# Optimization experiments

Measured on AMD Instinct MI355X. Metric: run time of the kernel, lower is better.

The kernel has to match this reference:

```python
import jax, jax.numpy as jnp
import numpy as np

TGT, BSZ, E, H, HD, P = 256, 64, 1024, 16, 64, 16
TAU = 3.0  # gumbel temperature
SCALE = 1.0 / np.sqrt(HD)


def setup_inputs() -> dict:
    rng = jax.random.key(0)
    ks = jax.random.split(rng, 14)
    n = lambda i, s: jax.random.normal(ks[i], s, dtype=jnp.float32)
    u = jax.random.uniform(ks[7], (BSZ, 2), dtype=jnp.float32, minval=1e-6, maxval=1.0 - 1e-6)
    return {
        'idx': 0,
        'query': n(0, (TGT, BSZ, E)),
        'key': n(1, (TGT, BSZ, E)),
        'value': n(2, (TGT, BSZ, E)),
        'prefix': n(3, (BSZ, 2, P, E)) * 0.5,  # gathered prefix_pool[prompt_ids]
        'batch_weight': jax.random.uniform(ks[4], (BSZ,), dtype=jnp.float32),
        'ori_image_features': n(5, (BSZ, 512)),
        'gumbel_noise': -jnp.log(-jnp.log(u)),  # standard gumbel(0,1) noise
        'in_proj_w': n(8, (3 * E, E)) * 0.02,
        'in_proj_b': jnp.zeros((3 * E,), jnp.float32),
        'out_w': n(9, (E, E)) * 0.02,
        'out_b': jnp.zeros((E,), jnp.float32),
        'gumbel_w': n(10, (2, 512)) * 0.05,
        'gumbel_b': jnp.zeros((2,), jnp.float32),
    }


def _sdpa(q, k, v):
    # q:[b,h,t,d] k,v:[b,h,s,d]
    s = jnp.einsum('bhtd,bhsd->bhts', q, k) * SCALE
    a = jax.nn.softmax(s, axis=-1)
    return jnp.einsum('bhts,bhsd->bhtd', a, v)


def reference(idx, query, key, value, prefix, batch_weight, ori_image_features,
              gumbel_noise, in_proj_w, in_proj_b, out_w, out_b, gumbel_w, gumbel_b):
    tgt, bsz, e = query.shape
    src = key.shape[0]
    # packed in-projection (w chunked into q/k/v blocks)
    w_q, w_k, w_v = jnp.split(in_proj_w, 3, axis=0)
    b_q, b_k, b_v = jnp.split(in_proj_b, 3, axis=0)
    q = query @ w_q.T + b_q            # [t,b,E]
    k = key @ w_k.T + b_k              # [s,b,E]
    v = value @ w_v.T + b_v
    # -> [b,h,t,d]
    q = q.reshape(tgt, bsz, H, HD).transpose(1, 2, 0, 3)
    k = k.reshape(src, bsz, H, HD).transpose(1, 2, 0, 3)
    v = v.reshape(src, bsz, H, HD).transpose(1, 2, 0, 3)
    # prefix k/v: [b,P,E] -> [b,h,P,d] (no in-projection, used raw as in source)
    pk = prefix[:, 0].reshape(bsz, P, H, HD).transpose(0, 2, 1, 3)
    pv = prefix[:, 1].reshape(bsz, P, H, HD).transpose(0, 2, 1, 3)

    attn = _sdpa(q, k, v)                      # [b,h,t,d]
    attn_flat = attn.transpose(2, 0, 1, 3).reshape(tgt * bsz, e)  # (t,b) row order

    attn_pre = _sdpa(q, pk, pv) * batch_weight[:, None, None, None]
    attn_pre_flat = attn_pre.transpose(2, 0, 1, 3).reshape(tgt * bsz, e)

    # gumbel-softmax gate (soft), one 2-way gate per sample
    logits = ori_image_features @ gumbel_w.T + gumbel_b           # [b,2]
    gumbel = jax.nn.softmax((logits + gumbel_noise) / TAU, axis=-1)
    gate = jnp.repeat(gumbel, tgt, axis=0)                        # [b*t,2] (b,t) order, as in source
    combined = attn_flat * gate[:, :1] + (attn_flat + attn_pre_flat) * gate[:, 1:2]

    out = combined @ out_w.T + out_b
    return out.reshape(tgt, bsz, e)
```

## Files before the change

kernel.cpp:

```cpp
#include <hip/hip_runtime.h>

typedef __attribute__((ext_vector_type(8))) short bf16x8;
typedef __attribute__((ext_vector_type(4))) float f32x4;
typedef __attribute__((ext_vector_type(8))) unsigned short ushort8;
typedef __attribute__((ext_vector_type(4))) unsigned short ushort4v;
typedef __attribute__((ext_vector_type(4))) float float4v;
typedef __attribute__((ext_vector_type(2))) unsigned int uint2v;

#define TGT 256
#define BSZ 64
#define EMB 1024
#define NH 16
#define HD 64
#define PP 16

__device__ __forceinline__ float b2f(unsigned short u) {
  return __builtin_bit_cast(float, ((unsigned int)u) << 16);
}
__device__ __forceinline__ unsigned short f2b(float f) {
  unsigned int u = __builtin_bit_cast(unsigned int, f);
  u += 0x7fffu + ((u >> 16) & 1u);
  return (unsigned short)(u >> 16);
}
__device__ __forceinline__ unsigned int pack2(float lo, float hi) {
  return (unsigned int)f2b(lo) | ((unsigned int)f2b(hi) << 16);
}
__device__ __forceinline__ f32x4 mfma16(bf16x8 a, bf16x8 b, f32x4 c) {
  return __builtin_amdgcn_mfma_f32_16x16x32_bf16(a, b, c, 0, 0, 0);
}
__device__ __forceinline__ void gl_lds16(const unsigned short* g, unsigned short* l) {
  __builtin_amdgcn_global_load_lds(
      (const __attribute__((address_space(1))) unsigned int*)g,
      (__attribute__((address_space(3))) unsigned int*)l, 16, 0, 0);
}

__global__ __launch_bounds__(64) void gate_kernel(
    const float* __restrict__ feat, const float* __restrict__ gw,
    const float* __restrict__ gb, const float* __restrict__ noise,
    float* __restrict__ g1) {
  const int b = blockIdx.x, lane = threadIdx.x;
  float a0 = 0.f, a1 = 0.f;
  for (int i = lane; i < 512; i += 64) {
    float f = feat[b * 512 + i];
    a0 += f * gw[i];
    a1 += f * gw[512 + i];
  }
#pragma unroll
  for (int off = 32; off >= 1; off >>= 1) {
    a0 += __shfl_xor(a0, off);
    a1 += __shfl_xor(a1, off);
  }
  if (lane == 0) {
    float l0 = (a0 + gb[0] + noise[b * 2 + 0]) * (1.0f / 3.0f);
    float l1 = (a1 + gb[1] + noise[b * 2 + 1]) * (1.0f / 3.0f);
    float mm = fmaxf(l0, l1);
    float e0 = __expf(l0 - mm), e1 = __expf(l1 - mm);
    g1[b] = e1 / (e0 + e1);
  }
}

__global__ __launch_bounds__(256) void cast_bf16_kernel(
    const float* __restrict__ in, unsigned short* __restrict__ out, int n8) {
  int i = blockIdx.x * blockDim.x + threadIdx.x;
  const int stride = gridDim.x * blockDim.x;
  for (; i < n8; i += stride) {
    const float4v* p = (const float4v*)(in + (size_t)i * 8);
    float4v v0 = p[0], v1 = p[1];
    ushort8 o = {f2b(v0[0]), f2b(v0[1]), f2b(v0[2]), f2b(v0[3]),
                 f2b(v1[0]), f2b(v1[1]), f2b(v1[2]), f2b(v1[3])};
    *(ushort8*)(out + (size_t)i * 8) = o;
  }
}

#define STAGE_A(s)                                       \
  {                                                      \
    int k0s = (s) * 32;                                  \
    unsigned short* d = &As[(s) & 3][wl];                \
    gl_lds16(a0p + k0s, d);                              \
    gl_lds16(a1p + k0s, d + 4096);                       \
  }
#define STAGE_B(s)                                       \
  {                                                      \
    int k0s = (s) * 32;                                  \
    unsigned short* d = &Bs[(s) & 3][wl];                \
    gl_lds16(b0p + k0s, d);                              \
    gl_lds16(b1p + k0s, d + 4096);                       \
  }
#define GEMM_STEP(s, DO_STAGE)                                        \
  {                                                                   \
    const unsigned short* Ab = &As[(s) & 3][0];                       \
    const unsigned short* Bb = &Bs[(s) & 3][0];                       \
    bf16x8 af[8], bfr[4];                                             \
    _Pragma("unroll") for (int mi = 0; mi < 8; ++mi)                  \
        af[mi] = *(const bf16x8*)&Ab[aoff + mi * 512];                \
    _Pragma("unroll") for (int ni = 0; ni < 2; ++ni)                  \
        bfr[ni] = *(const bf16x8*)&Bb[boff + ni * 512];               \
    if (DO_STAGE) STAGE_A((s) + 3);                                   \
    __builtin_amdgcn_s_barrier();                                     \
    __builtin_amdgcn_s_setprio(1);                                    \
    _Pragma("unroll") for (int mi = 0; mi < 8; ++mi) {                \
      acc[mi][0] = mfma16(af[mi], bfr[0], acc[mi][0]);                \
      acc[mi][1] = mfma16(af[mi], bfr[1], acc[mi][1]);                \
    }                                                                 \
    __builtin_amdgcn_s_setprio(0);                                    \
    __builtin_amdgcn_s_barrier();                                     \
    _Pragma("unroll") for (int ni = 2; ni < 4; ++ni)                  \
        bfr[ni] = *(const bf16x8*)&Bb[boff + ni * 512];               \
    if (DO_STAGE) STAGE_B((s) + 3);                                   \
    __builtin_amdgcn_s_barrier();                                     \
    __builtin_amdgcn_s_setprio(1);                                    \
    _Pragma("unroll") for (int mi = 0; mi < 8; ++mi) {                \
      acc[mi][2] = mfma16(af[mi], bfr[2], acc[mi][2]);                \
      acc[mi][3] = mfma16(af[mi], bfr[3], acc[mi][3]);                \
    }                                                                 \
    __builtin_amdgcn_s_setprio(0);                                    \
  }
#define STEP_WAIT(cntstr)                                \
  asm volatile("s_waitcnt " cntstr ::: "memory");        \
  __builtin_amdgcn_sched_barrier(0);                     \
  __builtin_amdgcn_s_barrier();

template <int OUT_F32, int QSCALE>
__global__ __launch_bounds__(512, 2) void gemm256_kernel(
    const unsigned short* __restrict__ A, const unsigned short* __restrict__ W,
    const float* __restrict__ bias, void* __restrict__ Cv) {
  constexpr int K = 1024, N = 1024;
  __shared__ __attribute__((aligned(16))) unsigned short As[4][8192];
  __shared__ __attribute__((aligned(16))) unsigned short Bs[4][8192];
  const int tid = threadIdx.x;
  const int wv = tid >> 6, lane = tid & 63;
  const int l15 = lane & 15, kg = lane >> 4;
  const int bid = blockIdx.x;
  const int cpx = gridDim.x >> 3;
  const int wg = (bid & 7) * cpx + (bid >> 3);
  const int m0 = (wg >> 2) * 256, n0 = (wg & 3) * 256;
  const int wmL = (wv >> 2) * 128, wnL = (wv & 3) * 64;

  const int sr = wv * 16 + (lane >> 2);
  const int sc = ((lane & 3) * 8) ^ (((sr >> 1) & 3) << 3);
  const unsigned short* a0p = A + (size_t)(m0 + sr) * K + sc;
  const unsigned short* a1p = a0p + (size_t)128 * K;
  const unsigned short* b0p = W + (size_t)(n0 + sr) * K + sc;
  const unsigned short* b1p = b0p + (size_t)128 * K;
  const int wl = wv * 512;

  const int x = ((l15 >> 1) & 3) << 3;
  const int aoff = (wmL + l15) * 32 + ((kg * 8) ^ x);
  const int boff = (wnL + l15) * 32 + ((kg * 8) ^ x);

  f32x4 acc[8][4];
#pragma unroll
  for (int i = 0; i < 8; ++i)
#pragma unroll
    for (int j = 0; j < 4; ++j) acc[i][j] = (f32x4){0.f, 0.f, 0.f, 0.f};

  STAGE_A(0); STAGE_B(0); STAGE_A(1); STAGE_B(1); STAGE_A(2); STAGE_B(2);
  STEP_WAIT("vmcnt(8)")

  for (int s = 0; s < 29; ++s) {
    GEMM_STEP(s, 1);
    STEP_WAIT("vmcnt(8)")
  }
  GEMM_STEP(29, 0);
  STEP_WAIT("vmcnt(4)")
  GEMM_STEP(30, 0);
  STEP_WAIT("vmcnt(0)")
  GEMM_STEP(31, 0);

#pragma unroll
  for (int mi = 0; mi < 8; ++mi) {
#pragma unroll
    for (int ni = 0; ni < 4; ++ni) {
      int col = n0 + wnL + ni * 16 + l15;
      float bcol = bias[col];
#pragma unroll
      for (int r = 0; r < 4; ++r) {
        int row = m0 + wmL + mi * 16 + kg * 4 + r;
        float v = acc[mi][ni][r] + bcol;
        if constexpr (QSCALE) v *= 0.125f;
        if constexpr (OUT_F32)
          ((float*)Cv)[(size_t)row * N + col] = v;
        else
          ((unsigned short*)Cv)[(size_t)row * N + col] = f2b(v);
      }
    }
  }
}

__global__ __launch_bounds__(512) void attn_kernel(
    const unsigned short* __restrict__ qb, const unsigned short* __restrict__ kb,
    const unsigned short* __restrict__ vb, const float* __restrict__ prefix,
    const float* __restrict__ bw, const float* __restrict__ g1,
    unsigned short* __restrict__ comb) {
  const int b = blockIdx.x, h = blockIdx.y;
  __shared__ __attribute__((aligned(16))) unsigned short Kl[256][64];
  __shared__ __attribute__((aligned(16))) unsigned short Vt[64 * 256];
  __shared__ __attribute__((aligned(16))) unsigned short PKl[16][64];
  __shared__ __attribute__((aligned(16))) unsigned short PVt[64][32];
  __shared__ __attribute__((aligned(16))) unsigned short Plds[8][16][40];
  unsigned short* Cb = &Kl[0][0];
  const int tid = threadIdx.x;

#pragma unroll
  for (int it = 0; it < 4; ++it) {
    int cid = tid + it * 512;
    int j = cid >> 3, c = cid & 7;
    size_t gro = (size_t)(j * BSZ + b) * EMB + h * HD + c * 8;
    *(ushort8*)&Kl[j][((c ^ (j & 7)) << 3)] = *(const ushort8*)(kb + gro);
    ushort8 vv = *(const ushort8*)(vb + gro);
#pragma unroll
    for (int i = 0; i < 8; ++i)
      Vt[(c * 8 + i) * 256 + (((j >> 3) ^ i) << 3) + (j & 7)] = vv[i];
  }
  if (tid < 256) {
    int arr = tid >> 7, cid = tid & 127;
    int sp = cid >> 3, c = cid & 7;
    const float* src = prefix + ((size_t)(b * 2 + arr) * PP + sp) * EMB + h * HD + c * 8;
    float4v v0 = *(const float4v*)src;
    float4v v1 = *(const float4v*)(src + 4);
    if (arr == 0) {
      ushort8 o = {f2b(v0[0]), f2b(v0[1]), f2b(v0[2]), f2b(v0[3]),
                   f2b(v1[0]), f2b(v1[1]), f2b(v1[2]), f2b(v1[3])};
      *(ushort8*)&PKl[sp][((c ^ (sp & 7)) << 3)] = o;
    } else {
#pragma unroll
      for (int i = 0; i < 8; ++i)
        PVt[c * 8 + i][sp] = f2b(i < 4 ? v0[i] : v1[i - 4]);
    }
  } else if (tid < 384) {
    int cid = tid - 256;
    *(ushort8*)&PVt[cid >> 1][16 + (cid & 1) * 8] = (ushort8){0, 0, 0, 0, 0, 0, 0, 0};
  }
  __syncthreads();

  const int wv = tid >> 6, lane = tid & 63;
  const int l15 = lane & 15, g = lane >> 4;
  const int swl = l15 & 7;
  const float bwb = bw[b];
  unsigned short(&Pw)[16][40] = Plds[wv];
  f32x4 Oacc[2][4];

#pragma unroll
  for (int sI = 0; sI < 2; ++sI) {
    const int tg = wv * 32 + sI * 16 + l15;
    const size_t qoff = (size_t)(tg * BSZ + b) * EMB + h * HD;
    bf16x8 qf0 = *(const bf16x8*)(qb + qoff + g * 8);
    bf16x8 qf1 = *(const bf16x8*)(qb + qoff + 32 + g * 8);
    f32x4 O[4];
#pragma unroll
    for (int dt = 0; dt < 4; ++dt) O[dt] = (f32x4){0.f, 0.f, 0.f, 0.f};
    float m = -3.0e38f, l = 0.f;

#pragma unroll
    for (int ch = 0; ch < 8; ++ch) {
      const int rA = ch * 32 + l15, rB = rA + 16;
      bf16x8 ka0 = *(const bf16x8*)&Kl[rA][((g ^ swl) << 3)];
      bf16x8 ka1 = *(const bf16x8*)&Kl[rA][(((4 + g) ^ swl) << 3)];
      bf16x8 kb0 = *(const bf16x8*)&Kl[rB][((g ^ swl) << 3)];
      bf16x8 kb1 = *(const bf16x8*)&Kl[rB][(((4 + g) ^ swl) << 3)];
      f32x4 sa = (f32x4){0.f, 0.f, 0.f, 0.f}, sb = sa;
      sa = mfma16(ka0, qf0, sa);
      sa = mfma16(ka1, qf1, sa);
      sb = mfma16(kb0, qf0, sb);
      sb = mfma16(kb1, qf1, sb);
      float mx = fmaxf(fmaxf(fmaxf(sa[0], sa[1]), fmaxf(sa[2], sa[3])),
                       fmaxf(fmaxf(sb[0], sb[1]), fmaxf(sb[2], sb[3])));
      mx = fmaxf(mx, __shfl_xor(mx, 16));
      mx = fmaxf(mx, __shfl_xor(mx, 32));
      float mn = fmaxf(m, mx);
      float f = __expf(m - mn);
      m = mn;
      float pA[4], pB[4];
#pragma unroll
      for (int r = 0; r < 4; ++r) {
        pA[r] = __expf(sa[r] - m);
        pB[r] = __expf(sb[r] - m);
      }
      uint2v wa = {pack2(pA[0], pA[1]), pack2(pA[2], pA[3])};
      uint2v wb2 = {pack2(pB[0], pB[1]), pack2(pB[2], pB[3])};
      *(uint2v*)&Pw[l15][g * 4] = wa;
      *(uint2v*)&Pw[l15][16 + g * 4] = wb2;
      float sloc = b2f((unsigned short)(wa[0] & 0xffff)) + b2f((unsigned short)(wa[0] >> 16)) +
                   b2f((unsigned short)(wa[1] & 0xffff)) + b2f((unsigned short)(wa[1] >> 16)) +
                   b2f((unsigned short)(wb2[0] & 0xffff)) + b2f((unsigned short)(wb2[0] >> 16)) +
                   b2f((unsigned short)(wb2[1] & 0xffff)) + b2f((unsigned short)(wb2[1] >> 16));
      l = l * f + sloc;
#pragma unroll
      for (int dt = 0; dt < 4; ++dt)
#pragma unroll
        for (int r = 0; r < 4; ++r) O[dt][r] *= f;
      bf16x8 pf = *(const bf16x8*)&Pw[l15][g * 8];
#pragma unroll
      for (int dt = 0; dt < 4; ++dt) {
        const int drow = dt * 16 + l15;
        bf16x8 vf = *(const bf16x8*)&Vt[drow * 256 + (((ch * 4 + g) ^ (drow & 7)) << 3)];
        O[dt] = mfma16(vf, pf, O[dt]);
      }
    }

    float lf = l;
    lf += __shfl_xor(lf, 16);
    lf += __shfl_xor(lf, 32);
    float inv = 1.0f / lf;
#pragma unroll
    for (int dt = 0; dt < 4; ++dt)
#pragma unroll
      for (int r = 0; r < 4; ++r) O[dt][r] *= inv;

    bf16x8 pk0 = *(const bf16x8*)&PKl[l15][((g ^ swl) << 3)];
    bf16x8 pk1 = *(const bf16x8*)&PKl[l15][(((4 + g) ^ swl) << 3)];
    f32x4 sp4 = (f32x4){0.f, 0.f, 0.f, 0.f};
    sp4 = mfma16(pk0, qf0, sp4);
    sp4 = mfma16(pk1, qf1, sp4);
    float pm = fmaxf(fmaxf(sp4[0], sp4[1]), fmaxf(sp4[2], sp4[3]));
    pm = fmaxf(pm, __shfl_xor(pm, 16));
    pm = fmaxf(pm, __shfl_xor(pm, 32));
    float pe[4], pl = 0.f;
#pragma unroll
    for (int r = 0; r < 4; ++r) {
      pe[r] = __expf(sp4[r] - pm);
      pl += pe[r];
    }
    pl += __shfl_xor(pl, 16);
    pl += __shfl_xor(pl, 32);
    float cpre = g1[tg >> 2] * bwb / pl;
#pragma unroll
    for (int r = 0; r < 4; ++r) pe[r] *= cpre;
    *(uint2v*)&Pw[l15][g * 4] = (uint2v){pack2(pe[0], pe[1]), pack2(pe[2], pe[3])};
    *(uint2v*)&Pw[l15][16 + g * 4] = (uint2v){0u, 0u};
    bf16x8 ppf = *(const bf16x8*)&Pw[l15][g * 8];
#pragma unroll
    for (int dt = 0; dt < 4; ++dt) {
      bf16x8 pvf = *(const bf16x8*)&PVt[dt * 16 + l15][g * 8];
      O[dt] = mfma16(pvf, ppf, O[dt]);
    }
#pragma unroll
    for (int dt = 0; dt < 4; ++dt) Oacc[sI][dt] = O[dt];
  }

  __syncthreads();
#pragma unroll
  for (int sI = 0; sI < 2; ++sI) {
    int t = wv * 32 + sI * 16 + l15;
#pragma unroll
    for (int dt = 0; dt < 4; ++dt) {
#pragma unroll
      for (int u = 0; u < 2; ++u) {
        unsigned int pw = pack2(Oacc[sI][dt][2 * u], Oacc[sI][dt][2 * u + 1]);
        int d = dt * 16 + g * 4 + 2 * u;
        *(unsigned int*)&Cb[t * 64 + (((d >> 3) ^ (t & 7)) << 3) + (d & 7)] = pw;
      }
    }
  }
  __syncthreads();
#pragma unroll
  for (int it = 0; it < 4; ++it) {
    int cid = tid + it * 512;
    int j = cid >> 3, c = cid & 7;
    ushort8 row = *(const ushort8*)&Cb[j * 64 + ((c ^ (j & 7)) << 3)];
    *(ushort8*)(comb + (size_t)(j * BSZ + b) * EMB + h * HD + c * 8) = row;
  }
}

extern "C" void kernel_launch(void* const* d_in, const int* in_sizes, int n_in,
                              void* d_out, int out_size, void* d_ws, size_t ws_size,
                              hipStream_t stream) {
  const float* query = (const float*)d_in[1];
  const float* key = (const float*)d_in[2];
  const float* value = (const float*)d_in[3];
  const float* prefix = (const float*)d_in[4];
  const float* bw = (const float*)d_in[5];
  const float* feat = (const float*)d_in[6];
  const float* noise = (const float*)d_in[7];
  const float* ipw = (const float*)d_in[8];
  const float* ipb = (const float*)d_in[9];
  const float* outw = (const float*)d_in[10];
  const float* outb = (const float*)d_in[11];
  const float* gw = (const float*)d_in[12];
  const float* gb = (const float*)d_in[13];
  float* out = (float*)d_out;

  char* ws = (char*)d_ws;
  const size_t MATB = (size_t)16384 * 1024;
  unsigned short* qb = (unsigned short*)ws;
  unsigned short* kb = qb + MATB;
  unsigned short* vb = kb + MATB;
  unsigned short* cb = vb + MATB;
  unsigned short* wip = cb + MATB;
  unsigned short* wo = wip + (size_t)3072 * 1024;
  float* g1 = (float*)(wo + (size_t)1024 * 1024);

  gate_kernel<<<64, 64, 0, stream>>>(feat, gw, gb, noise, g1);

  cast_bf16_kernel<<<1536, 256, 0, stream>>>(ipw, wip, 3072 * 1024 / 8);
  cast_bf16_kernel<<<512, 256, 0, stream>>>(outw, wo, 1024 * 1024 / 8);

  const int N8 = (int)(MATB / 8);
  cast_bf16_kernel<<<2048, 256, 0, stream>>>(query, cb, N8);
  gemm256_kernel<0, 1><<<256, 512, 0, stream>>>(cb, wip, ipb, qb);
  cast_bf16_kernel<<<2048, 256, 0, stream>>>(key, cb, N8);
  gemm256_kernel<0, 0><<<256, 512, 0, stream>>>(cb, wip + (size_t)1024 * 1024, ipb + 1024, kb);
  cast_bf16_kernel<<<2048, 256, 0, stream>>>(value, cb, N8);
  gemm256_kernel<0, 0><<<256, 512, 0, stream>>>(cb, wip + (size_t)2048 * 1024, ipb + 2048, vb);

  attn_kernel<<<dim3(64, 16), 512, 0, stream>>>(qb, kb, vb, prefix, bw, g1, cb);

  gemm256_kernel<1, 0><<<256, 512, 0, stream>>>(cb, wo, outb, out);
}
```

Baseline: 295.3 us.

## Interleave two query tiles per wave, lazy softmax rescale, re-swizzle V transpose

Each wave now processes its two 16-row query tiles together inside the key-chunk loop. The K fragments and V fragments loaded from LDS are reused by both tiles, halving LDS reads and adding independent MFMA work per iteration. The online softmax rescale is skipped unless the new max exceeds the running max by more than 8, which avoids multiplying the accumulators on most chunks. The risk is that the unnormalized exponentials can grow up to e^8 before bf16 packing. The V transpose swizzle also gains an extra XOR term to reduce LDS bank conflicts on stores and loads.

```diff
diff --git a/kernel.cpp b/kernel.cpp
--- a/kernel.cpp
+++ b/kernel.cpp
@@ -209,8 +209,10 @@
     *(ushort8*)&Kl[j][((c ^ (j & 7)) << 3)] = *(const ushort8*)(kb + gro);
     ushort8 vv = *(const ushort8*)(vb + gro);
 #pragma unroll
-    for (int i = 0; i < 8; ++i)
-      Vt[(c * 8 + i) * 256 + (((j >> 3) ^ i) << 3) + (j & 7)] = vv[i];
+    for (int i = 0; i < 8; ++i) {
+      int gran = (j >> 3) ^ i ^ c;
+      Vt[(c * 8 + i) * 256 + gran * 8 + (j & 7)] = vv[i];
+    }
   }
   if (tid < 256) {
     int arr = tid >> 7, cid = tid & 127;
@@ -238,43 +240,63 @@
   const int swl = l15 & 7;
   const float bwb = bw[b];
   unsigned short(&Pw)[16][40] = Plds[wv];
-  f32x4 Oacc[2][4];
-
-#pragma unroll
-  for (int sI = 0; sI < 2; ++sI) {
-    const int tg = wv * 32 + sI * 16 + l15;
-    const size_t qoff = (size_t)(tg * BSZ + b) * EMB + h * HD;
-    bf16x8 qf0 = *(const bf16x8*)(qb + qoff + g * 8);
-    bf16x8 qf1 = *(const bf16x8*)(qb + qoff + 32 + g * 8);
-    f32x4 O[4];
-#pragma unroll
-    for (int dt = 0; dt < 4; ++dt) O[dt] = (f32x4){0.f, 0.f, 0.f, 0.f};
-    float m = -3.0e38f, l = 0.f;
-
-#pragma unroll
-    for (int ch = 0; ch < 8; ++ch) {
-      const int rA = ch * 32 + l15, rB = rA + 16;
-      bf16x8 ka0 = *(const bf16x8*)&Kl[rA][((g ^ swl) << 3)];
-      bf16x8 ka1 = *(const bf16x8*)&Kl[rA][(((4 + g) ^ swl) << 3)];
-      bf16x8 kb0 = *(const bf16x8*)&Kl[rB][((g ^ swl) << 3)];
-      bf16x8 kb1 = *(const bf16x8*)&Kl[rB][(((4 + g) ^ swl) << 3)];
-      f32x4 sa = (f32x4){0.f, 0.f, 0.f, 0.f}, sb = sa;
-      sa = mfma16(ka0, qf0, sa);
-      sa = mfma16(ka1, qf1, sa);
-      sb = mfma16(kb0, qf0, sb);
-      sb = mfma16(kb1, qf1, sb);
+
+  const int t0 = wv * 32 + l15;
+  const size_t qo0 = (size_t)(t0 * BSZ + b) * EMB + h * HD;
+  const size_t qo1 = (size_t)((t0 + 16) * BSZ + b) * EMB + h * HD;
+  bf16x8 qf[2][2];
+  qf[0][0] = *(const bf16x8*)(qb + qo0 + g * 8);
+  qf[0][1] = *(const bf16x8*)(qb + qo0 + 32 + g * 8);
+  qf[1][0] = *(const bf16x8*)(qb + qo1 + g * 8);
+  qf[1][1] = *(const bf16x8*)(qb + qo1 + 32 + g * 8);
+
+  f32x4 O[2][4];
+#pragma unroll
+  for (int st = 0; st < 2; ++st)
+#pragma unroll
+    for (int dt = 0; dt < 4; ++dt) O[st][dt] = (f32x4){0.f, 0.f, 0.f, 0.f};
+  float m[2] = {-3.0e38f, -3.0e38f}, l[2] = {0.f, 0.f};
+
+#pragma unroll
+  for (int ch = 0; ch < 8; ++ch) {
+    const int rA = ch * 32 + l15, rB = rA + 16;
+    bf16x8 ka0 = *(const bf16x8*)&Kl[rA][((g ^ swl) << 3)];
+    bf16x8 ka1 = *(const bf16x8*)&Kl[rA][(((4 + g) ^ swl) << 3)];
+    bf16x8 kb0 = *(const bf16x8*)&Kl[rB][((g ^ swl) << 3)];
+    bf16x8 kb1 = *(const bf16x8*)&Kl[rB][(((4 + g) ^ swl) << 3)];
+    f32x4 s[2][2];
+#pragma unroll
+    for (int st = 0; st < 2; ++st) {
+      s[st][0] = (f32x4){0.f, 0.f, 0.f, 0.f};
+      s[st][1] = (f32x4){0.f, 0.f, 0.f, 0.f};
+      s[st][0] = mfma16(ka0, qf[st][0], s[st][0]);
+      s[st][0] = mfma16(ka1, qf[st][1], s[st][0]);
+      s[st][1] = mfma16(kb0, qf[st][0], s[st][1]);
+      s[st][1] = mfma16(kb1, qf[st][1], s[st][1]);
+    }
+    bf16x8 pf[2];
+#pragma unroll
+    for (int st = 0; st < 2; ++st) {
+      f32x4 sa = s[st][0], sb = s[st][1];
       float mx = fmaxf(fmaxf(fmaxf(sa[0], sa[1]), fmaxf(sa[2], sa[3])),
                        fmaxf(fmaxf(sb[0], sb[1]), fmaxf(sb[2], sb[3])));
       mx = fmaxf(mx, __shfl_xor(mx, 16));
       mx = fmaxf(mx, __shfl_xor(mx, 32));
-      float mn = fmaxf(m, mx);
-      float f = __expf(m - mn);
-      m = mn;
+      if (__ballot(mx > m[st] + 8.0f) != 0ull) {
+        float mn = fmaxf(m[st], mx);
+        float f = __expf(m[st] - mn);
+        m[st] = mn;
+        l[st] *= f;
+#pragma unroll
+        for (int dt = 0; dt < 4; ++dt)
+#pragma unroll
+          for (int r = 0; r < 4; ++r) O[st][dt][r] *= f;
+      }
       float pA[4], pB[4];
 #pragma unroll
       for (int r = 0; r < 4; ++r) {
-        pA[r] = __expf(sa[r] - m);
-        pB[r] = __expf(sb[r] - m);
+        pA[r] = __expf(sa[r] - m[st]);
+        pB[r] = __expf(sb[r] - m[st]);
       }
       uint2v wa = {pack2(pA[0], pA[1]), pack2(pA[2], pA[3])};
       uint2v wb2 = {pack2(pB[0], pB[1]), pack2(pB[2], pB[3])};
@@ -284,69 +306,75 @@
                    b2f((unsigned short)(wa[1] & 0xffff)) + b2f((unsigned short)(wa[1] >> 16)) +
                    b2f((unsigned short)(wb2[0] & 0xffff)) + b2f((unsigned short)(wb2[0] >> 16)) +
                    b2f((unsigned short)(wb2[1] & 0xffff)) + b2f((unsigned short)(wb2[1] >> 16));
-      l = l * f + sloc;
-#pragma unroll
-      for (int dt = 0; dt < 4; ++dt)
-#pragma unroll
-        for (int r = 0; r < 4; ++r) O[dt][r] *= f;
-      bf16x8 pf = *(const bf16x8*)&Pw[l15][g * 8];
-#pragma unroll
-      for (int dt = 0; dt < 4; ++dt) {
-        const int drow = dt * 16 + l15;
-        bf16x8 vf = *(const bf16x8*)&Vt[drow * 256 + (((ch * 4 + g) ^ (drow & 7)) << 3)];
-        O[dt] = mfma16(vf, pf, O[dt]);
-      }
-    }
-
-    float lf = l;
+      l[st] += sloc;
+      pf[st] = *(const bf16x8*)&Pw[l15][g * 8];
+    }
+#pragma unroll
+    for (int dt = 0; dt < 4; ++dt) {
+      const int drow = dt * 16 + l15;
+      const int gran = (ch * 4 + g) ^ (drow & 7) ^ (drow >> 3);
+      bf16x8 vf = *(const bf16x8*)&Vt[drow * 256 + gran * 8];
+      O[0][dt] = mfma16(vf, pf[0], O[0][dt]);
+      O[1][dt] = mfma16(vf, pf[1], O[1][dt]);
+    }
+  }
+
+#pragma unroll
+  for (int st = 0; st < 2; ++st) {
+    float lf = l[st];
     lf += __shfl_xor(lf, 16);
     lf += __shfl_xor(lf, 32);
     float inv = 1.0f / lf;
 #pragma unroll
     for (int dt = 0; dt < 4; ++dt)
 #pragma unroll
-      for (int r = 0; r < 4; ++r) O[dt][r] *= inv;
-
+      for (int r = 0; r < 4; ++r) O[st][dt][r] *= inv;
+  }
+
+  {
     bf16x8 pk0 = *(const bf16x8*)&PKl[l15][((g ^ swl) << 3)];
     bf16x8 pk1 = *(const bf16x8*)&PKl[l15][(((4 + g) ^ swl) << 3)];
-    f32x4 sp4 = (f32x4){0.f, 0.f, 0.f, 0.f};
-    sp4 = mfma16(pk0, qf0, sp4);
-    sp4 = mfma16(pk1, qf1, sp4);
-    float pm = fmaxf(fmaxf(sp4[0], sp4[1]), fmaxf(sp4[2], sp4[3]));
-    pm = fmaxf(pm, __shfl_xor(pm, 16));
-    pm = fmaxf(pm, __shfl_xor(pm, 32));
-    float pe[4], pl = 0.f;
-#pragma unroll
-    for (int r = 0; r < 4; ++r) {
-      pe[r] = __expf(sp4[r] - pm);
-      pl += pe[r];
-    }
-    pl += __shfl_xor(pl, 16);
-    pl += __shfl_xor(pl, 32);
-    float cpre = g1[tg >> 2] * bwb / pl;
-#pragma unroll
-    for (int r = 0; r < 4; ++r) pe[r] *= cpre;
-    *(uint2v*)&Pw[l15][g * 4] = (uint2v){pack2(pe[0], pe[1]), pack2(pe[2], pe[3])};
-    *(uint2v*)&Pw[l15][16 + g * 4] = (uint2v){0u, 0u};
-    bf16x8 ppf = *(const bf16x8*)&Pw[l15][g * 8];
+    bf16x8 ppf[2];
+#pragma unroll
+    for (int st = 0; st < 2; ++st) {
+      f32x4 sp4 = (f32x4){0.f, 0.f, 0.f, 0.f};
+      sp4 = mfma16(pk0, qf[st][0], sp4);
+      sp4 = mfma16(pk1, qf[st][1], sp4);
+      float pm = fmaxf(fmaxf(sp4[0], sp4[1]), fmaxf(sp4[2], sp4[3]));
+      pm = fmaxf(pm, __shfl_xor(pm, 16));
+      pm = fmaxf(pm, __shfl_xor(pm, 32));
+      float pe[4], pl = 0.f;
+#pragma unroll
+      for (int r = 0; r < 4; ++r) {
+        pe[r] = __expf(sp4[r] - pm);
+        pl += pe[r];
+      }
+      pl += __shfl_xor(pl, 16);
+      pl += __shfl_xor(pl, 32);
+      float cpre = g1[(t0 + 16 * st) >> 2] * bwb / pl;
+#pragma unroll
+      for (int r = 0; r < 4; ++r) pe[r] *= cpre;
+      *(uint2v*)&Pw[l15][g * 4] = (uint2v){pack2(pe[0], pe[1]), pack2(pe[2], pe[3])};
+      *(uint2v*)&Pw[l15][16 + g * 4] = (uint2v){0u, 0u};
+      ppf[st] = *(const bf16x8*)&Pw[l15][g * 8];
+    }
 #pragma unroll
     for (int dt = 0; dt < 4; ++dt) {
       bf16x8 pvf = *(const bf16x8*)&PVt[dt * 16 + l15][g * 8];
-      O[dt] = mfma16(pvf, ppf, O[dt]);
-    }
-#pragma unroll
-    for (int dt = 0; dt < 4; ++dt) Oacc[sI][dt] = O[dt];
+      O[0][dt] = mfma16(pvf, ppf[0], O[0][dt]);
+      O[1][dt] = mfma16(pvf, ppf[1], O[1][dt]);
+    }
   }
 
   __syncthreads();
 #pragma unroll
-  for (int sI = 0; sI < 2; ++sI) {
-    int t = wv * 32 + sI * 16 + l15;
+  for (int st = 0; st < 2; ++st) {
+    int t = wv * 32 + st * 16 + l15;
 #pragma unroll
     for (int dt = 0; dt < 4; ++dt) {
 #pragma unroll
       for (int u = 0; u < 2; ++u) {
-        unsigned int pw = pack2(Oacc[sI][dt][2 * u], Oacc[sI][dt][2 * u + 1]);
+        unsigned int pw = pack2(O[st][dt][2 * u], O[st][dt][2 * u + 1]);
         int d = dt * 16 + g * 4 + 2 * u;
         *(unsigned int*)&Cb[t * 64 + (((d >> 3) ^ (t & 7)) << 3) + (d & 7)] = pw;
       }
```

New measurement: 292.4 us. Within noise of the previous version (-1.0%).
